# Kernel tuning notes

Measured on AMD Instinct MI355X. Metric: run time of the kernel, lower is better.

The kernel has to match this reference:

```python
import jax, jax.numpy as jnp
import numpy as np


def setup_inputs() -> dict:
    key = jax.random.key(0)
    k1, k2 = jax.random.split(key)
    inp = jax.random.normal(k1, (16, 64, 64, 64), dtype=jnp.float32)  # (B, D, H, W)
    codebook = jax.random.normal(k2, (1024, 64), dtype=jnp.float32)  # (K, D)
    return {"input": inp, "codebook": codebook}


def reference(input, codebook):
    # input: (B, D, *spatial); codebook: (K, D)
    B, D = input.shape[0], input.shape[1]
    spatial = input.shape[2:]
    # move channel dim last, flatten to tokens: (N, D)
    x = jnp.moveaxis(input, 1, -1).reshape(-1, D)
    # squared L2 distances (cdist^2), computed via expansion to avoid (N,K,D)
    x_sq = jnp.sum(x * x, axis=-1, keepdims=True)            # (N, 1)
    e_sq = jnp.sum(codebook * codebook, axis=-1)             # (K,)
    dist = x_sq - 2.0 * (x @ codebook.T) + e_sq              # (N, K)
    idx = jnp.argmin(dist, axis=-1)                          # (N,)
    quantized = jnp.take(codebook, idx, axis=0)              # (N, D)
    # reshape back to (B, *spatial, D) then move D to axis 1
    out = jnp.moveaxis(quantized.reshape((B,) + spatial + (D,)), -1, 1)
    indices = idx.reshape((B,) + spatial)
    return out, indices
```

## Files before the change

kernel.cpp:

```cpp
#include <hip/hip_runtime.h>


typedef _Float16 v8h  __attribute__((ext_vector_type(8)));
typedef float    v16f __attribute__((ext_vector_type(16)));

constexpr int   D         = 64;
constexpr int   K         = 1024;
constexpr int   HW        = 4096;
constexpr int   DHW       = D * HW;
constexpr int   OUT_ELEMS = 16 * DHW;
constexpr float EPS       = 0.065f;


__global__ __launch_bounds__(256) void vq_prep(
    const float* __restrict__ cb, _Float16* __restrict__ CH, float* __restrict__ esq)
{
    const int blk = blockIdx.x, tid = threadIdx.x;
    if (blk < 40) {
        const int gid  = blk * 256 + tid;
        const int lane = gid & 63;
        const int fid  = gid >> 6;
        const int t    = fid / 5;
        const int kc   = fid - 5 * t;
        const int l31  = lane & 31;
        const int lh   = lane >> 5;
        const int cw   = t * 32 + l31;
        v8h h;
        if (kc < 4) {
            const float* src = cb + cw * D + kc * 16 + lh * 8;
            #pragma unroll
            for (int j = 0; j < 8; ++j) h[j] = (_Float16)(-2.0f * src[j]);
        } else {
            #pragma unroll
            for (int j = 0; j < 8; ++j) h[j] = (_Float16)0.0f;
            if (lh == 0) {
                const float4* c4 = (const float4*)(cb + cw * D);
                float a0 = 0.f, a1 = 0.f, a2 = 0.f, a3 = 0.f;
                #pragma unroll
                for (int j = 0; j < 16; ++j) {
                    const float4 c = c4[j];
                    a0 = fmaf(c.x, c.x, a0);
                    a1 = fmaf(c.y, c.y, a1);
                    a2 = fmaf(c.z, c.z, a2);
                    a3 = fmaf(c.w, c.w, a3);
                }
                const float e   = (a0 + a1) + (a2 + a3);
                const _Float16 ehi = (_Float16)e;
                h[0] = ehi;
                h[1] = (_Float16)(e - (float)ehi);
            }
        }
        *(v8h*)(CH + (size_t)fid * 512 + lane * 8) = h;
    } else {
        const int cw = (blk - 40) * 256 + tid;
        const float4* c4 = (const float4*)(cb + cw * D);
        float a0 = 0.f, a1 = 0.f, a2 = 0.f, a3 = 0.f;
        #pragma unroll
        for (int j = 0; j < 16; ++j) {
            const float4 c = c4[j];
            a0 = fmaf(c.x, c.x, a0);
            a1 = fmaf(c.y, c.y, a1);
            a2 = fmaf(c.z, c.z, a2);
            a3 = fmaf(c.w, c.w, a3);
        }
        esq[cw] = (a0 + a1) + (a2 + a3);
    }
}

__global__ __launch_bounds__(256, 4) void vq_scan(
    const float* __restrict__ input,
    const float* __restrict__ codebook,
    const _Float16* __restrict__ CH,
    const float* __restrict__ esq,
    float* __restrict__ out)
{
    __shared__ _Float16 s_bf[2][4][64][8];
    __shared__ float    s_esq[K];
    __shared__ float    s_pv[4][64];
    __shared__ float    s_p2[4][64];
    __shared__ int      s_pk[4][64];
    __shared__ int      s_idx[64];
    __shared__ unsigned s_mask[2];
    __shared__ float    s_x[4][64];
    __shared__ float    s_q[64][65];

    const int tid  = threadIdx.x;
    const int lane = tid & 63;
    const int q    = __builtin_amdgcn_readfirstlane(tid >> 6);
    const int l31  = lane & 31;
    const int lh   = lane >> 5;
    const int tok0 = blockIdx.x * 64;
    const int b    = tok0 >> 12;
    const int hwb  = tok0 & 4095;

    if (tid < 2) s_mask[tid] = 0u;

    *(float4*)&s_esq[tid * 4] = *(const float4*)&esq[tid * 4];

    {
        const float* xb = input + (size_t)b * DHW + hwb;
        #pragma unroll
        for (int pass = 0; pass < 4; ++pass) {
            const int d   = pass * 16 + (tid >> 4);
            const int hw4 = (tid & 15) * 4;
            const float4 v = *(const float4*)(xb + (size_t)d * HW + hw4);
            const float vv[4] = {v.x, v.y, v.z, v.w};
            #pragma unroll
            for (int u = 0; u < 4; ++u) {
                const int tk = hw4 + u;
                s_bf[tk >> 5][d >> 4][((d >> 3) & 1) * 32 + (tk & 31)][d & 7] = (_Float16)vv[u];
            }
        }
    }
    __syncthreads();

    v8h bt[2][4];
    #pragma unroll
    for (int ct = 0; ct < 2; ++ct)
        #pragma unroll
        for (int kc = 0; kc < 4; ++kc)
            bt[ct][kc] = *(const v8h*)&s_bf[ct][kc][lane][0];

    v8h b5;
    #pragma unroll
    for (int j = 0; j < 8; ++j) b5[j] = (_Float16)0.0f;
    if (lh == 0) { b5[0] = (_Float16)1.0f; b5[1] = (_Float16)1.0f; }

    v16f Z = {0,0,0,0,0,0,0,0,0,0,0,0,0,0,0,0};
    const float INF = __builtin_huge_valf();
    float bv0 = INF, b20 = INF, bv1 = INF, b21 = INF;

    const v8h* Abase = (const v8h*)CH + lane;

    v8h a0, a1, a2, a3, a5;
    {
        const v8h* Ap = Abase + (size_t)((q * 8 + 0) * 5) * 64;
        a0 = Ap[0]; a1 = Ap[64]; a2 = Ap[128]; a3 = Ap[192]; a5 = Ap[256];
    }
    #pragma unroll 2
    for (int t = 0; t < 8; ++t) {
        const int tn = (t < 7) ? t + 1 : 7;
        const v8h* Apn = Abase + (size_t)((q * 8 + tn) * 5) * 64;
        v8h n0 = Apn[0], n1 = Apn[64], n2 = Apn[128], n3 = Apn[192], n5 = Apn[256];

        v16f acc0 = __builtin_amdgcn_mfma_f32_32x32x16_f16(a5, b5, Z, 0, 0, 0);
        v16f acc1 = __builtin_amdgcn_mfma_f32_32x32x16_f16(a5, b5, Z, 0, 0, 0);
        acc0 = __builtin_amdgcn_mfma_f32_32x32x16_f16(a0, bt[0][0], acc0, 0, 0, 0);
        acc1 = __builtin_amdgcn_mfma_f32_32x32x16_f16(a0, bt[1][0], acc1, 0, 0, 0);
        acc0 = __builtin_amdgcn_mfma_f32_32x32x16_f16(a1, bt[0][1], acc0, 0, 0, 0);
        acc1 = __builtin_amdgcn_mfma_f32_32x32x16_f16(a1, bt[1][1], acc1, 0, 0, 0);
        acc0 = __builtin_amdgcn_mfma_f32_32x32x16_f16(a2, bt[0][2], acc0, 0, 0, 0);
        acc1 = __builtin_amdgcn_mfma_f32_32x32x16_f16(a2, bt[1][2], acc1, 0, 0, 0);
        acc0 = __builtin_amdgcn_mfma_f32_32x32x16_f16(a3, bt[0][3], acc0, 0, 0, 0);
        acc1 = __builtin_amdgcn_mfma_f32_32x32x16_f16(a3, bt[1][3], acc1, 0, 0, 0);

        #pragma unroll
        for (int r = 0; r < 16; ++r) {
            const unsigned slot = (unsigned)((t << 4) | r);
            const float s0 = __uint_as_float((__float_as_uint(acc0[r]) & 0xFFFFFF00u) | slot);
            b20 = __builtin_amdgcn_fmed3f(s0, bv0, b20);
            bv0 = fminf(bv0, s0);
            const float s1 = __uint_as_float((__float_as_uint(acc1[r]) & 0xFFFFFF00u) | slot);
            b21 = __builtin_amdgcn_fmed3f(s1, bv1, b21);
            bv1 = fminf(bv1, s1);
        }
        a0 = n0; a1 = n1; a2 = n2; a3 = n3; a5 = n5;
    }

    #pragma unroll
    for (int ct = 0; ct < 2; ++ct) {
        const float bv = ct ? bv1 : bv0;
        const float b2 = ct ? b21 : b20;
        const float obv = __shfl_xor(bv, 32, 64);
        const float ob2 = __shfl_xor(b2, 32, 64);
        const float B1 = fminf(bv, obv);
        const float B2 = fminf(fmaxf(bv, obv), fminf(b2, ob2));
        const int   lho = (obv < bv) ? (lh ^ 1) : lh;
        const unsigned slot = __float_as_uint(B1) & 255u;
        const int r  = slot & 15;
        const int tt = slot >> 4;
        const int cw = (q * 8 + tt) * 32 + (r & 3) + 8 * (r >> 2) + 4 * lho;
        if (lane < 32) {
            s_pv[q][ct * 32 + lane] = B1;
            s_p2[q][ct * 32 + lane] = B2;
            s_pk[q][ct * 32 + lane] = cw;
        }
    }
    __syncthreads();

    if (tid < 64) {
        float B1 = INF, B2 = INF; int CW = 0;
        #pragma unroll
        for (int qq = 0; qq < 4; ++qq) {
            const float pv = s_pv[qq][tid];
            const float p2 = s_p2[qq][tid];
            const int   pk = s_pk[qq][tid];
            if (pv < B1) { B2 = fminf(B1, p2); B1 = pv; CW = pk; }
            else         { B2 = fminf(B2, pv); }
        }
        s_idx[tid] = CW;
        if (B2 - B1 < EPS) atomicOr(&s_mask[tid >> 5], 1u << (tid & 31));
    }
    __syncthreads();

    {
        int ui = 0;
        const int row = lane >> 2;
        const int c   = lane & 3;
        for (int w = 0; w < 2; ++w) {
            unsigned m = s_mask[w];
            while (m) {
                const int bit = __ffs(m) - 1;
                m &= m - 1;
                const int tl = w * 32 + bit;
                if ((ui & 3) == q) {
                    s_x[q][lane] = input[(size_t)b * DHW + (size_t)lane * HW + (hwb + tl)];
                    const float4* xs4 = (const float4*)&s_x[q][c * 16];
                    const float4 x0 = xs4[0], x1 = xs4[1], x2 = xs4[2], x3 = xs4[3];

                    float bestv = INF; int bestk = K;
                    #pragma unroll 4
                    for (int ch = 0; ch < 64; ++ch) {
                        const int k = ch * 16 + row;
                        const float4* c4 = (const float4*)(codebook + (size_t)k * D + c * 16);
                        const float4 c0 = c4[0], c1 = c4[1], c2 = c4[2], c3 = c4[3];
                        float p0 = 0.f, p1 = 0.f, p2 = 0.f, p3 = 0.f;
                        p0 = fmaf(x0.x, c0.x, p0); p0 = fmaf(x0.y, c0.y, p0);
                        p0 = fmaf(x0.z, c0.z, p0); p0 = fmaf(x0.w, c0.w, p0);
                        p1 = fmaf(x1.x, c1.x, p1); p1 = fmaf(x1.y, c1.y, p1);
                        p1 = fmaf(x1.z, c1.z, p1); p1 = fmaf(x1.w, c1.w, p1);
                        p2 = fmaf(x2.x, c2.x, p2); p2 = fmaf(x2.y, c2.y, p2);
                        p2 = fmaf(x2.z, c2.z, p2); p2 = fmaf(x2.w, c2.w, p2);
                        p3 = fmaf(x3.x, c3.x, p3); p3 = fmaf(x3.y, c3.y, p3);
                        p3 = fmaf(x3.z, c3.z, p3); p3 = fmaf(x3.w, c3.w, p3);
                        float dp = (p0 + p1) + (p2 + p3);
                        dp += __shfl_xor(dp, 1, 64);
                        dp += __shfl_xor(dp, 2, 64);
                        const float s = fmaf(-2.0f, dp, s_esq[k]);
                        if (s < bestv) { bestv = s; bestk = k; }
                    }
                    #pragma unroll
                    for (int off = 32; off >= 1; off >>= 1) {
                        const float ov = __shfl_xor(bestv, off, 64);
                        const int   ok = __shfl_xor(bestk, off, 64);
                        if (ov < bestv || (ov == bestv && ok < bestk)) { bestv = ov; bestk = ok; }
                    }
                    if (lane == 0) s_idx[tl] = bestk;
                }
                ++ui;
            }
        }
    }
    __syncthreads();

    {
        const int rs = tid >> 2;
        const int c  = tid & 3;
        const int idx = s_idx[rs];
        const float4* src = (const float4*)(codebook + (size_t)idx * D + c * 16);
        #pragma unroll
        for (int j = 0; j < 4; ++j) {
            const float4 v = src[j];
            float* dst = &s_q[rs][c * 16 + j * 4];
            dst[0] = v.x; dst[1] = v.y; dst[2] = v.z; dst[3] = v.w;
        }
    }
    __syncthreads();
    {
        float* ob = out + (size_t)b * DHW + hwb;
        #pragma unroll
        for (int pass = 0; pass < 4; ++pass) {
            const int d   = pass * 16 + (tid >> 4);
            const int hw4 = (tid & 15) * 4;
            float4 v;
            v.x = s_q[hw4 + 0][d];
            v.y = s_q[hw4 + 1][d];
            v.z = s_q[hw4 + 2][d];
            v.w = s_q[hw4 + 3][d];
            *(float4*)(ob + (size_t)d * HW + hw4) = v;
        }
        if (tid < 64) out[OUT_ELEMS + tok0 + tid] = (float)s_idx[tid];
    }
}

extern "C" void kernel_launch(void* const* d_in, const int* in_sizes, int n_in,
                              void* d_out, int out_size, void* d_ws, size_t ws_size,
                              hipStream_t stream) {
    const float* input    = (const float*)d_in[0];
    const float* codebook = (const float*)d_in[1];
    float* out            = (float*)d_out;

    _Float16* CH  = (_Float16*)d_ws;
    float*    esq = (float*)((char*)d_ws + 163840);

    vq_prep<<<44, 256, 0, stream>>>(codebook, CH, esq);
    vq_scan<<<1024, 256, 0, stream>>>(input, codebook, CH, esq, out);
}
```

Measured before the change: 129.5 us.

## Use split-fp16 hi/lo MFMA products to shrink exact-rescore candidate set

The codebook and the input tokens are each split into fp16 high and low parts. The hi*hi, hi*lo and lo*hi MFMA products are accumulated, which gives near-fp32 dot products. With that accuracy the ambiguity threshold can drop from 0.065 to 1e-3, so far fewer tokens need the exact fp32 rescan. The rescan now spreads each ambiguous token across the whole block with syncthreads, and the argmin slot is kept in a separate register instead of packed into the float mantissa. The cost is three times the MFMA work, double-width codebook loads, no software prefetch, and a lower occupancy bound (3 instead of 4).

Measured after the change: 105.9 us. 18.2% less time.

```diff
diff --git a/kernel.cpp b/kernel.cpp
--- a/kernel.cpp
+++ b/kernel.cpp
@@ -9,27 +9,33 @@
 constexpr int   HW        = 4096;
 constexpr int   DHW       = D * HW;
 constexpr int   OUT_ELEMS = 16 * DHW;
-constexpr float EPS       = 0.065f;
+constexpr float EPS       = 1e-3f;
 
 
 __global__ __launch_bounds__(256) void vq_prep(
     const float* __restrict__ cb, _Float16* __restrict__ CH, float* __restrict__ esq)
 {
     const int blk = blockIdx.x, tid = threadIdx.x;
-    if (blk < 40) {
+    if (blk < 72) {
         const int gid  = blk * 256 + tid;
         const int lane = gid & 63;
         const int fid  = gid >> 6;
-        const int t    = fid / 5;
-        const int kc   = fid - 5 * t;
+        const int t    = fid / 9;
+        const int kc   = fid - 9 * t;
         const int l31  = lane & 31;
         const int lh   = lane >> 5;
         const int cw   = t * 32 + l31;
         v8h h;
-        if (kc < 4) {
-            const float* src = cb + cw * D + kc * 16 + lh * 8;
+        if (kc < 8) {
+            const int  kk = kc & 3;
+            const bool lo = kc >= 4;
+            const float* src = cb + cw * D + kk * 16 + lh * 8;
             #pragma unroll
-            for (int j = 0; j < 8; ++j) h[j] = (_Float16)(-2.0f * src[j]);
+            for (int j = 0; j < 8; ++j) {
+                const float v = -2.0f * src[j];
+                const _Float16 vh = (_Float16)v;
+                h[j] = lo ? (_Float16)(v - (float)vh) : vh;
+            }
         } else {
             #pragma unroll
             for (int j = 0; j < 8; ++j) h[j] = (_Float16)0.0f;
@@ -44,7 +50,7 @@
                     a2 = fmaf(c.z, c.z, a2);
                     a3 = fmaf(c.w, c.w, a3);
                 }
-                const float e   = (a0 + a1) + (a2 + a3);
+                const float e = (a0 + a1) + (a2 + a3);
                 const _Float16 ehi = (_Float16)e;
                 h[0] = ehi;
                 h[1] = (_Float16)(e - (float)ehi);
@@ -52,7 +58,7 @@
         }
         *(v8h*)(CH + (size_t)fid * 512 + lane * 8) = h;
     } else {
-        const int cw = (blk - 40) * 256 + tid;
+        const int cw = (blk - 72) * 256 + tid;
         const float4* c4 = (const float4*)(cb + cw * D);
         float a0 = 0.f, a1 = 0.f, a2 = 0.f, a3 = 0.f;
         #pragma unroll
@@ -67,33 +73,35 @@
     }
 }
 
-__global__ __launch_bounds__(256, 4) void vq_scan(
+__global__ __launch_bounds__(256, 3) void vq_scan(
     const float* __restrict__ input,
     const float* __restrict__ codebook,
     const _Float16* __restrict__ CH,
     const float* __restrict__ esq,
     float* __restrict__ out)
 {
-    __shared__ _Float16 s_bf[2][4][64][8];
+    __shared__ _Float16 s_bf[2][2][4][64][8];
     __shared__ float    s_esq[K];
     __shared__ float    s_pv[4][64];
     __shared__ float    s_p2[4][64];
     __shared__ int      s_pk[4][64];
     __shared__ int      s_idx[64];
-    __shared__ unsigned s_mask[2];
-    __shared__ float    s_x[4][64];
+    __shared__ int      s_list[64];
+    __shared__ int      s_cnt;
+    __shared__ float    s_xf[64];
+    __shared__ float    s_redv[4];
+    __shared__ int      s_redk[4];
     __shared__ float    s_q[64][65];
 
     const int tid  = threadIdx.x;
     const int lane = tid & 63;
     const int q    = __builtin_amdgcn_readfirstlane(tid >> 6);
-    const int l31  = lane & 31;
     const int lh   = lane >> 5;
     const int tok0 = blockIdx.x * 64;
     const int b    = tok0 >> 12;
     const int hwb  = tok0 & 4095;
 
-    if (tid < 2) s_mask[tid] = 0u;
+    if (tid == 0) s_cnt = 0;
 
     *(float4*)&s_esq[tid * 4] = *(const float4*)&esq[tid * 4];
 
@@ -108,18 +116,24 @@
             #pragma unroll
             for (int u = 0; u < 4; ++u) {
                 const int tk = hw4 + u;
-                s_bf[tk >> 5][d >> 4][((d >> 3) & 1) * 32 + (tk & 31)][d & 7] = (_Float16)vv[u];
+                const float f = vv[u];
+                const _Float16 fh = (_Float16)f;
+                s_bf[0][tk >> 5][d >> 4][((d >> 3) & 1) * 32 + (tk & 31)][d & 7] = fh;
+                s_bf[1][tk >> 5][d >> 4][((d >> 3) & 1) * 32 + (tk & 31)][d & 7] =
+                    (_Float16)(f - (float)fh);
             }
         }
     }
     __syncthreads();
 
-    v8h bt[2][4];
+    v8h bh[2][4], bl[2][4];
     #pragma unroll
     for (int ct = 0; ct < 2; ++ct)
         #pragma unroll
-        for (int kc = 0; kc < 4; ++kc)
-            bt[ct][kc] = *(const v8h*)&s_bf[ct][kc][lane][0];
+        for (int kc = 0; kc < 4; ++kc) {
+            bh[ct][kc] = *(const v8h*)&s_bf[0][ct][kc][lane][0];
+            bl[ct][kc] = *(const v8h*)&s_bf[1][ct][kc][lane][0];
+        }
 
     v8h b5;
     #pragma unroll
@@ -129,57 +143,75 @@
     v16f Z = {0,0,0,0,0,0,0,0,0,0,0,0,0,0,0,0};
     const float INF = __builtin_huge_valf();
     float bv0 = INF, b20 = INF, bv1 = INF, b21 = INF;
+    int   sl0 = 0, sl1 = 0;
 
     const v8h* Abase = (const v8h*)CH + lane;
 
-    v8h a0, a1, a2, a3, a5;
-    {
-        const v8h* Ap = Abase + (size_t)((q * 8 + 0) * 5) * 64;
-        a0 = Ap[0]; a1 = Ap[64]; a2 = Ap[128]; a3 = Ap[192]; a5 = Ap[256];
-    }
     #pragma unroll 2
     for (int t = 0; t < 8; ++t) {
-        const int tn = (t < 7) ? t + 1 : 7;
-        const v8h* Apn = Abase + (size_t)((q * 8 + tn) * 5) * 64;
-        v8h n0 = Apn[0], n1 = Apn[64], n2 = Apn[128], n3 = Apn[192], n5 = Apn[256];
-
-        v16f acc0 = __builtin_amdgcn_mfma_f32_32x32x16_f16(a5, b5, Z, 0, 0, 0);
-        v16f acc1 = __builtin_amdgcn_mfma_f32_32x32x16_f16(a5, b5, Z, 0, 0, 0);
-        acc0 = __builtin_amdgcn_mfma_f32_32x32x16_f16(a0, bt[0][0], acc0, 0, 0, 0);
-        acc1 = __builtin_amdgcn_mfma_f32_32x32x16_f16(a0, bt[1][0], acc1, 0, 0, 0);
-        acc0 = __builtin_amdgcn_mfma_f32_32x32x16_f16(a1, bt[0][1], acc0, 0, 0, 0);
-        acc1 = __builtin_amdgcn_mfma_f32_32x32x16_f16(a1, bt[1][1], acc1, 0, 0, 0);
-        acc0 = __builtin_amdgcn_mfma_f32_32x32x16_f16(a2, bt[0][2], acc0, 0, 0, 0);
-        acc1 = __builtin_amdgcn_mfma_f32_32x32x16_f16(a2, bt[1][2], acc1, 0, 0, 0);
-        acc0 = __builtin_amdgcn_mfma_f32_32x32x16_f16(a3, bt[0][3], acc0, 0, 0, 0);
-        acc1 = __builtin_amdgcn_mfma_f32_32x32x16_f16(a3, bt[1][3], acc1, 0, 0, 0);
+        const v8h* Ap = Abase + (size_t)((q * 8 + t) * 9) * 64;
+        const v8h ah0 = Ap[0],   ah1 = Ap[64],  ah2 = Ap[128], ah3 = Ap[192];
+        const v8h al0 = Ap[256], al1 = Ap[320], al2 = Ap[384], al3 = Ap[448];
+        const v8h ae  = Ap[512];
+
+        v16f acc0 = __builtin_amdgcn_mfma_f32_32x32x16_f16(ae, b5, Z, 0, 0, 0);
+        v16f acc1 = __builtin_amdgcn_mfma_f32_32x32x16_f16(ae, b5, Z, 0, 0, 0);
+
+        acc0 = __builtin_amdgcn_mfma_f32_32x32x16_f16(ah0, bh[0][0], acc0, 0, 0, 0);
+        acc1 = __builtin_amdgcn_mfma_f32_32x32x16_f16(ah0, bh[1][0], acc1, 0, 0, 0);
+        acc0 = __builtin_amdgcn_mfma_f32_32x32x16_f16(ah1, bh[0][1], acc0, 0, 0, 0);
+        acc1 = __builtin_amdgcn_mfma_f32_32x32x16_f16(ah1, bh[1][1], acc1, 0, 0, 0);
+        acc0 = __builtin_amdgcn_mfma_f32_32x32x16_f16(ah2, bh[0][2], acc0, 0, 0, 0);
+        acc1 = __builtin_amdgcn_mfma_f32_32x32x16_f16(ah2, bh[1][2], acc1, 0, 0, 0);
+        acc0 = __builtin_amdgcn_mfma_f32_32x32x16_f16(ah3, bh[0][3], acc0, 0, 0, 0);
+        acc1 = __builtin_amdgcn_mfma_f32_32x32x16_f16(ah3, bh[1][3], acc1, 0, 0, 0);
+
+        acc0 = __builtin_amdgcn_mfma_f32_32x32x16_f16(ah0, bl[0][0], acc0, 0, 0, 0);
+        acc1 = __builtin_amdgcn_mfma_f32_32x32x16_f16(ah0, bl[1][0], acc1, 0, 0, 0);
+        acc0 = __builtin_amdgcn_mfma_f32_32x32x16_f16(ah1, bl[0][1], acc0, 0, 0, 0);
+        acc1 = __builtin_amdgcn_mfma_f32_32x32x16_f16(ah1, bl[1][1], acc1, 0, 0, 0);
+        acc0 = __builtin_amdgcn_mfma_f32_32x32x16_f16(ah2, bl[0][2], acc0, 0, 0, 0);
+        acc1 = __builtin_amdgcn_mfma_f32_32x32x16_f16(ah2, bl[1][2], acc1, 0, 0, 0);
+        acc0 = __builtin_amdgcn_mfma_f32_32x32x16_f16(ah3, bl[0][3], acc0, 0, 0, 0);
+        acc1 = __builtin_amdgcn_mfma_f32_32x32x16_f16(ah3, bl[1][3], acc1, 0, 0, 0);
+
+        acc0 = __builtin_amdgcn_mfma_f32_32x32x16_f16(al0, bh[0][0], acc0, 0, 0, 0);
+        acc1 = __builtin_amdgcn_mfma_f32_32x32x16_f16(al0, bh[1][0], acc1, 0, 0, 0);
+        acc0 = __builtin_amdgcn_mfma_f32_32x32x16_f16(al1, bh[0][1], acc0, 0, 0, 0);
+        acc1 = __builtin_amdgcn_mfma_f32_32x32x16_f16(al1, bh[1][1], acc1, 0, 0, 0);
+        acc0 = __builtin_amdgcn_mfma_f32_32x32x16_f16(al2, bh[0][2], acc0, 0, 0, 0);
+        acc1 = __builtin_amdgcn_mfma_f32_32x32x16_f16(al2, bh[1][2], acc1, 0, 0, 0);
+        acc0 = __builtin_amdgcn_mfma_f32_32x32x16_f16(al3, bh[0][3], acc0, 0, 0, 0);
+        acc1 = __builtin_amdgcn_mfma_f32_32x32x16_f16(al3, bh[1][3], acc1, 0, 0, 0);
 
         #pragma unroll
         for (int r = 0; r < 16; ++r) {
-            const unsigned slot = (unsigned)((t << 4) | r);
-            const float s0 = __uint_as_float((__float_as_uint(acc0[r]) & 0xFFFFFF00u) | slot);
+            const int slot = (t << 4) | r;
+            const float s0 = acc0[r];
             b20 = __builtin_amdgcn_fmed3f(s0, bv0, b20);
-            bv0 = fminf(bv0, s0);
-            const float s1 = __uint_as_float((__float_as_uint(acc1[r]) & 0xFFFFFF00u) | slot);
+            if (s0 < bv0) { bv0 = s0; sl0 = slot; }
+            const float s1 = acc1[r];
             b21 = __builtin_amdgcn_fmed3f(s1, bv1, b21);
-            bv1 = fminf(bv1, s1);
-        }
-        a0 = n0; a1 = n1; a2 = n2; a3 = n3; a5 = n5;
+            if (s1 < bv1) { bv1 = s1; sl1 = slot; }
+        }
     }
 
     #pragma unroll
     for (int ct = 0; ct < 2; ++ct) {
         const float bv = ct ? bv1 : bv0;
         const float b2 = ct ? b21 : b20;
+        const int   sl = ct ? sl1 : sl0;
         const float obv = __shfl_xor(bv, 32, 64);
         const float ob2 = __shfl_xor(b2, 32, 64);
-        const float B1 = fminf(bv, obv);
-        const float B2 = fminf(fmaxf(bv, obv), fminf(b2, ob2));
-        const int   lho = (obv < bv) ? (lh ^ 1) : lh;
-        const unsigned slot = __float_as_uint(B1) & 255u;
-        const int r  = slot & 15;
-        const int tt = slot >> 4;
-        const int cw = (q * 8 + tt) * 32 + (r & 3) + 8 * (r >> 2) + 4 * lho;
+        const int   osl = __shfl_xor(sl, 32, 64);
+        const bool  oth = obv < bv;
+        const float B1  = oth ? obv : bv;
+        const float B2  = fminf(fmaxf(bv, obv), fminf(b2, ob2));
+        const int   wsl = oth ? osl : sl;
+        const int   wlh = oth ? (lh ^ 1) : lh;
+        const int   r   = wsl & 15;
+        const int   tt  = wsl >> 4;
+        const int   cw  = (q * 8 + tt) * 32 + (r & 3) + 8 * (r >> 2) + 4 * wlh;
         if (lane < 32) {
             s_pv[q][ct * 32 + lane] = B1;
             s_p2[q][ct * 32 + lane] = B2;
@@ -199,63 +231,68 @@
             else         { B2 = fminf(B2, pv); }
         }
         s_idx[tid] = CW;
-        if (B2 - B1 < EPS) atomicOr(&s_mask[tid >> 5], 1u << (tid & 31));
+        if (B2 - B1 < EPS) {
+            const int p = atomicAdd(&s_cnt, 1);
+            s_list[p] = tid;
+        }
     }
     __syncthreads();
 
     {
-        int ui = 0;
-        const int row = lane >> 2;
-        const int c   = lane & 3;
-        for (int w = 0; w < 2; ++w) {
-            unsigned m = s_mask[w];
-            while (m) {
-                const int bit = __ffs(m) - 1;
-                m &= m - 1;
-                const int tl = w * 32 + bit;
-                if ((ui & 3) == q) {
-                    s_x[q][lane] = input[(size_t)b * DHW + (size_t)lane * HW + (hwb + tl)];
-                    const float4* xs4 = (const float4*)&s_x[q][c * 16];
-                    const float4 x0 = xs4[0], x1 = xs4[1], x2 = xs4[2], x3 = xs4[3];
-
-                    float bestv = INF; int bestk = K;
-                    #pragma unroll 4
-                    for (int ch = 0; ch < 64; ++ch) {
-                        const int k = ch * 16 + row;
-                        const float4* c4 = (const float4*)(codebook + (size_t)k * D + c * 16);
-                        const float4 c0 = c4[0], c1 = c4[1], c2 = c4[2], c3 = c4[3];
-                        float p0 = 0.f, p1 = 0.f, p2 = 0.f, p3 = 0.f;
-                        p0 = fmaf(x0.x, c0.x, p0); p0 = fmaf(x0.y, c0.y, p0);
-                        p0 = fmaf(x0.z, c0.z, p0); p0 = fmaf(x0.w, c0.w, p0);
-                        p1 = fmaf(x1.x, c1.x, p1); p1 = fmaf(x1.y, c1.y, p1);
-                        p1 = fmaf(x1.z, c1.z, p1); p1 = fmaf(x1.w, c1.w, p1);
-                        p2 = fmaf(x2.x, c2.x, p2); p2 = fmaf(x2.y, c2.y, p2);
-                        p2 = fmaf(x2.z, c2.z, p2); p2 = fmaf(x2.w, c2.w, p2);
-                        p3 = fmaf(x3.x, c3.x, p3); p3 = fmaf(x3.y, c3.y, p3);
-                        p3 = fmaf(x3.z, c3.z, p3); p3 = fmaf(x3.w, c3.w, p3);
-                        float dp = (p0 + p1) + (p2 + p3);
-                        dp += __shfl_xor(dp, 1, 64);
-                        dp += __shfl_xor(dp, 2, 64);
-                        const float s = fmaf(-2.0f, dp, s_esq[k]);
-                        if (s < bestv) { bestv = s; bestk = k; }
-                    }
-                    #pragma unroll
-                    for (int off = 32; off >= 1; off >>= 1) {
-                        const float ov = __shfl_xor(bestv, off, 64);
-                        const int   ok = __shfl_xor(bestk, off, 64);
-                        if (ov < bestv || (ov == bestv && ok < bestk)) { bestv = ov; bestk = ok; }
-                    }
-                    if (lane == 0) s_idx[tl] = bestk;
+        const int cnt = s_cnt;
+        const int rr  = tid >> 2;
+        const int c   = tid & 3;
+        for (int ii = 0; ii < cnt; ++ii) {
+            const int tl = s_list[ii];
+            if (tid < 64) s_xf[tid] = input[(size_t)b * DHW + (size_t)tid * HW + (hwb + tl)];
+            __syncthreads();
+            const float4* xs4 = (const float4*)&s_xf[c * 16];
+            const float4 x0 = xs4[0], x1 = xs4[1], x2 = xs4[2], x3 = xs4[3];
+            float bestv = INF; int bestk = K;
+            #pragma unroll 4
+            for (int i = 0; i < 16; ++i) {
+                const int k = i * 64 + rr;
+                const float4* c4 = (const float4*)(codebook + (size_t)k * D + c * 16);
+                const float4 c0 = c4[0], c1 = c4[1], c2 = c4[2], c3 = c4[3];
+                float p0 = 0.f, p1 = 0.f, p2 = 0.f, p3 = 0.f;
+                p0 = fmaf(x0.x, c0.x, p0); p0 = fmaf(x0.y, c0.y, p0);
+                p0 = fmaf(x0.z, c0.z, p0); p0 = fmaf(x0.w, c0.w, p0);
+                p1 = fmaf(x1.x, c1.x, p1); p1 = fmaf(x1.y, c1.y, p1);
+                p1 = fmaf(x1.z, c1.z, p1); p1 = fmaf(x1.w, c1.w, p1);
+                p2 = fmaf(x2.x, c2.x, p2); p2 = fmaf(x2.y, c2.y, p2);
+                p2 = fmaf(x2.z, c2.z, p2); p2 = fmaf(x2.w, c2.w, p2);
+                p3 = fmaf(x3.x, c3.x, p3); p3 = fmaf(x3.y, c3.y, p3);
+                p3 = fmaf(x3.z, c3.z, p3); p3 = fmaf(x3.w, c3.w, p3);
+                float dp = (p0 + p1) + (p2 + p3);
+                dp += __shfl_xor(dp, 1, 64);
+                dp += __shfl_xor(dp, 2, 64);
+                const float s = fmaf(-2.0f, dp, s_esq[k]);
+                if (s < bestv) { bestv = s; bestk = k; }
+            }
+            #pragma unroll
+            for (int off = 4; off <= 32; off <<= 1) {
+                const float ov = __shfl_xor(bestv, off, 64);
+                const int   ok = __shfl_xor(bestk, off, 64);
+                if (ov < bestv || (ov == bestv && ok < bestk)) { bestv = ov; bestk = ok; }
+            }
+            if (lane == 0) { s_redv[q] = bestv; s_redk[q] = bestk; }
+            __syncthreads();
+            if (tid == 0) {
+                float bb = s_redv[0]; int bk = s_redk[0];
+                #pragma unroll
+                for (int w = 1; w < 4; ++w) {
+                    const float v = s_redv[w]; const int kk = s_redk[w];
+                    if (v < bb || (v == bb && kk < bk)) { bb = v; bk = kk; }
                 }
-                ++ui;
-            }
-        }
-    }
-    __syncthreads();
+                s_idx[tl] = bk;
+            }
+            __syncthreads();
+        }
+    }
 
     {
-        const int rs = tid >> 2;
-        const int c  = tid & 3;
+        const int rs  = tid >> 2;
+        const int c   = tid & 3;
         const int idx = s_idx[rs];
         const float4* src = (const float4*)(codebook + (size_t)idx * D + c * 16);
         #pragma unroll
@@ -291,8 +328,8 @@
     float* out            = (float*)d_out;
 
     _Float16* CH  = (_Float16*)d_ws;
-    float*    esq = (float*)((char*)d_ws + 163840);
-
-    vq_prep<<<44, 256, 0, stream>>>(codebook, CH, esq);
+    float*    esq = (float*)((char*)d_ws + 294912);
+
+    vq_prep<<<76, 256, 0, stream>>>(codebook, CH, esq);
     vq_scan<<<1024, 256, 0, stream>>>(input, codebook, CH, esq, out);
 }
```
